# Optimization experiments

Measured on AMD Instinct MI355X. Metric: run time of the kernel, lower is better.

## Reference

```python
import jax, jax.numpy as jnp
import numpy as np

SIZE = 32            # resize target from size=(32,32)
CAL_THRESH = 0.3
WIN = 11             # standard SSIM gaussian window
SIGMA = 1.5
C1 = (0.01 * 255.0) ** 2   # data range 255 (patches are raw pixel values)
C2 = (0.03 * 255.0) ** 2


def _gauss_window():
    g = np.exp(-((np.arange(WIN) - WIN // 2) ** 2) / (2.0 * SIGMA ** 2))
    g = g / g.sum()
    return jnp.asarray(np.outer(g, g), jnp.float32)


def _gconv(x, win):
    # depthwise gaussian blur, same padding; x: [N,C,H,W]
    C = x.shape[1]
    k = jnp.tile(win[None, None], (C, 1, 1, 1))
    return jax.lax.conv_general_dilated(
        x, k, (1, 1), 'SAME',
        dimension_numbers=('NCHW', 'OIHW', 'NCHW'), feature_group_count=C)


def _crop_resize(img, box):
    # img: [C,H,W]; box: [x,y,w,h] with (x,y) = top-left (as used by the crop).
    # Equivalent to img[:, int(y):int(y+h), int(x):int(x+w)] then bilinear
    # F.interpolate to (SIZE,SIZE), align_corners=False (edge-clamped).
    C, H, W = img.shape
    x0 = jnp.floor(box[0]); y0 = jnp.floor(box[1])
    w = jnp.floor(box[0] + box[2]) - x0   # int(x+w) - int(x)
    h = jnp.floor(box[1] + box[3]) - y0
    ys = jnp.clip((jnp.arange(SIZE, dtype=jnp.float32) + 0.5) * (h / SIZE) - 0.5,
                  0.0, jnp.maximum(h - 1.0, 0.0))
    xs = jnp.clip((jnp.arange(SIZE, dtype=jnp.float32) + 0.5) * (w / SIZE) - 0.5,
                  0.0, jnp.maximum(w - 1.0, 0.0))
    yf = jnp.floor(ys); xf = jnp.floor(xs)
    wy = (ys - yf)[None, :, None]   # row weights
    wx = (xs - xf)[None, None, :]   # col weights

    def gi(yi, xi):
        yi = jnp.clip(yi, 0, H - 1).astype(jnp.int32)
        xi = jnp.clip(xi, 0, W - 1).astype(jnp.int32)
        return img[:, yi[:, None], xi[None, :]]  # [C,SIZE,SIZE]

    ylo = yf + y0; yhi = jnp.minimum(yf + 1.0, jnp.maximum(h - 1.0, 0.0)) + y0
    xlo = xf + x0; xhi = jnp.minimum(xf + 1.0, jnp.maximum(w - 1.0, 0.0)) + x0
    top = gi(ylo, xlo) * (1.0 - wx) + gi(ylo, xhi) * wx
    bot = gi(yhi, xlo) * (1.0 - wx) + gi(yhi, xhi) * wx
    return top * (1.0 - wy) + bot * wy


def _pairwise_iou(gt, pr):
    # faithful to get_two_box_iou: (x,y) treated as CENTER here (source quirk)
    g = gt[:, :, None, :]; p = pr[:, None, :, :]
    tl = jnp.maximum(g[..., :2] - g[..., 2:] / 2, p[..., :2] - p[..., 2:] / 2)
    br = jnp.minimum(g[..., :2] + g[..., 2:] / 2, p[..., :2] + p[..., 2:] / 2)
    en = jnp.prod((tl < br).astype(gt.dtype), axis=-1)
    area_i = jnp.prod(br - tl, axis=-1) * en
    area_g = jnp.prod(gt[..., 2:], axis=-1)[:, :, None]
    area_p = jnp.prod(pr[..., 2:], axis=-1)[:, None, :]
    return area_i / (area_g + area_p - area_i + 1e-16)  # [B,G,P]


def setup_inputs() -> dict:
    key = jax.random.key(0)
    k1, k2, k3, k4, k5 = jax.random.split(key, 5)
    B, G, P, H, W = 8, 16, 64, 640, 640
    imgs = jax.random.uniform(k1, (B, 3, H, W), jnp.float32) * 255.0
    xy = jax.random.uniform(k2, (B, G, 2), jnp.float32) * (W - 80.0) + 4.0
    wh = jax.random.uniform(k3, (B, G, 2), jnp.float32) * 56.0 + 8.0
    gt_boxes = jnp.concatenate([xy, wh], axis=-1)
    base = jnp.tile(gt_boxes, (1, P // G, 1))  # preds jittered around GTs so IoU>thresh often
    jit_xy = jax.random.uniform(k4, (B, P, 2), jnp.float32, -4.0, 4.0)
    jit_wh = jax.random.uniform(k5, (B, P, 2), jnp.float32, -4.0, 4.0)
    pred_boxes = jnp.concatenate(
        [base[..., :2] + jit_xy, jnp.maximum(base[..., 2:] + jit_wh, 3.0)], axis=-1)
    return {"gt_boxes": gt_boxes, "pred_boxes": pred_boxes, "imgs": imgs}


def reference(gt_boxes, pred_boxes, imgs):
    B, G = gt_boxes.shape[:2]; P = pred_boxes.shape[1]
    crop = jax.vmap(jax.vmap(_crop_resize, in_axes=(None, 0)), in_axes=(0, 0))
    gt_patch = crop(imgs, gt_boxes)     # [B,G,3,S,S]
    pr_patch = crop(imgs, pred_boxes)   # [B,P,3,S,S]

    iou = _pairwise_iou(gt_boxes, pred_boxes)                    # [B,G,P]
    valid = (pred_boxes[..., 2] > 2) & (pred_boxes[..., 3] > 2)  # [B,P]
    mask = ((iou > CAL_THRESH) & valid[:, None, :]).astype(imgs.dtype)

    # surviving pairs -> dense pair grid (masked mean == mean over survivors)
    x = jnp.broadcast_to(pr_patch[:, None], (B, G, P, 3, SIZE, SIZE)).reshape(-1, 3, SIZE, SIZE)
    y = jnp.broadcast_to(gt_patch[:, :, None], (B, G, P, 3, SIZE, SIZE)).reshape(-1, 3, SIZE, SIZE)

    win = _gauss_window()
    mu1 = _gconv(x, win); mu2 = _gconv(y, win)
    mu1_sq = mu1 * mu1; mu2_sq = mu2 * mu2; mu12 = mu1 * mu2
    s1 = _gconv(x * x, win) - mu1_sq
    s2 = _gconv(y * y, win) - mu2_sq
    s12 = _gconv(x * y, win) - mu12
    ssim_map = ((2 * mu12 + C1) * (2 * s12 + C2)) / ((mu1_sq + mu2_sq + C1) * (s1 + s2 + C2))

    loss = jnp.abs(x / 255.0 - y / 255.0) + (1.0 - ssim_map)    # L1 + SSIM loss, [N,3,S,S]
    loss = loss.reshape(B, G, P, 3, SIZE, SIZE)
    m = mask[:, :, :, None, None, None]
    cnt = jnp.sum(mask) * (3 * SIZE * SIZE)
    total = jnp.sum(loss * m)
    return jnp.where(cnt > 0, total / jnp.maximum(cnt, 1.0), 0.0)
```

## Files before the change

kernel.cpp:

```cpp
#include <hip/hip_runtime.h>
#include <math.h>

#define TSIZE 32
#define WIN 11
#define NB 8
#define NG 16
#define NP 64
#define IMH 640
#define IMW 640
#define NBOX 640
#define NPAIR 8192

#define C1F 6.5025f
#define C2F 58.5225f

struct GaussW { float g[WIN]; };
struct f4 { float v[4]; };

__global__ __launch_bounds__(256) void gen_patches(
    const float* __restrict__ gt_boxes, const float* __restrict__ pred_boxes,
    const float* __restrict__ imgs,
    float* __restrict__ patches, float* __restrict__ mus, float* __restrict__ gsqs,
    int* __restrict__ pair_list, int* __restrict__ pair_cnt, GaussW gw)
{
    const int bid = blockIdx.x;
    const int tid = threadIdx.x;

    if (bid >= NBOX * 3) {
        const int p = (bid - NBOX * 3) * 256 + tid;
        const int b  = p >> 10;
        const int gi = (p >> 6) & 15;
        const int pi = p & 63;
        bool mask;
        {
#pragma clang fp contract(off)
            const float* gb = gt_boxes  + ((size_t)b * NG + gi) * 4;
            const float* pb = pred_boxes + ((size_t)b * NP + pi) * 4;
            const float gx = gb[0], gy = gb[1], gw_ = gb[2], gh = gb[3];
            const float px = pb[0], py = pb[1], pw = pb[2], ph = pb[3];
            const float tlx = fmaxf(gx - gw_ / 2.0f, px - pw / 2.0f);
            const float tly = fmaxf(gy - gh / 2.0f, py - ph / 2.0f);
            const float brx = fminf(gx + gw_ / 2.0f, px + pw / 2.0f);
            const float bry = fminf(gy + gh / 2.0f, py + ph / 2.0f);
            const float en = ((tlx < brx) ? 1.0f : 0.0f) * ((tly < bry) ? 1.0f : 0.0f);
            const float ai = ((brx - tlx) * (bry - tly)) * en;
            const float ag = gw_ * gh;
            const float ap = pw * ph;
            const float iou = ai / (ag + ap - ai + 1e-16f);
            mask = (iou > 0.3f) && (pw > 2.0f) && (ph > 2.0f);
        }
        if (mask) {
            const int slot = atomicAdd(pair_cnt, 1);
            pair_list[slot] = p;
        }
        return;
    }

    const int box = bid / 3;
    const int c   = bid - box * 3;
    int b;
    const float* boxp;
    if (box < NB * NG) {
        b = box >> 4;
        boxp = gt_boxes + (size_t)box * 4;
    } else {
        const int q = box - NB * NG;
        b = q >> 6;
        boxp = pred_boxes + (size_t)q * 4;
    }
    const float* __restrict__ ic = imgs + ((size_t)b * 3 + c) * (IMH * IMW);
    float* __restrict__ patch_o = patches + ((size_t)box * 3 + c) * 1024;
    float* __restrict__ mu_o    = mus     + ((size_t)box * 3 + c) * 1024;
    float* __restrict__ gsq_o   = gsqs    + ((size_t)box * 3 + c) * 1024;

    __shared__ int   s_ylo[TSIZE], s_yhi[TSIZE], s_xlo[TSIZE], s_xhi[TSIZE];
    __shared__ float s_wy[TSIZE], s_wx[TSIZE];
    __shared__ float sp[1024], ta[1024], tb[1024];

    {
#pragma clang fp contract(off)
        const float b0 = boxp[0], b1 = boxp[1], b2 = boxp[2], b3 = boxp[3];
        const float x0 = floorf(b0), y0 = floorf(b1);
        const float w = floorf(b0 + b2) - x0;
        const float h = floorf(b1 + b3) - y0;

        if (tid < TSIZE) {
            const int t = tid;
            const float hm = fmaxf(h - 1.0f, 0.0f);
            const float scale = h / 32.0f;
            float ys = ((float)t + 0.5f) * scale - 0.5f;
            ys = fminf(fmaxf(ys, 0.0f), hm);
            const float yf = floorf(ys);
            s_wy[t] = ys - yf;
            const float ylo = yf + y0;
            const float yhi = fminf(yf + 1.0f, hm) + y0;
            s_ylo[t] = (int)fminf(fmaxf(ylo, 0.0f), (float)(IMH - 1));
            s_yhi[t] = (int)fminf(fmaxf(yhi, 0.0f), (float)(IMH - 1));
        } else if (tid < 2 * TSIZE) {
            const int t = tid - TSIZE;
            const float wm = fmaxf(w - 1.0f, 0.0f);
            const float scale = w / 32.0f;
            float xs = ((float)t + 0.5f) * scale - 0.5f;
            xs = fminf(fmaxf(xs, 0.0f), wm);
            const float xf = floorf(xs);
            s_wx[t] = xs - xf;
            const float xlo = xf + x0;
            const float xhi = fminf(xf + 1.0f, wm) + x0;
            s_xlo[t] = (int)fminf(fmaxf(xlo, 0.0f), (float)(IMW - 1));
            s_xhi[t] = (int)fminf(fmaxf(xhi, 0.0f), (float)(IMW - 1));
        }
    }
    __syncthreads();

    const int i  = tid >> 3;
    const int j4 = (tid & 7) << 2;
    const int e4 = (i << 5) + j4;

    {
        const int ylo = s_ylo[i], yhi = s_yhi[i];
        const float wy = s_wy[i];
        float vv[4];
#pragma unroll
        for (int q = 0; q < 4; ++q) {
#pragma clang fp contract(off)
            const int j = j4 + q;
            const int xlo = s_xlo[j], xhi = s_xhi[j];
            const float wx = s_wx[j];
            const float tl = ic[ylo * IMW + xlo], tr = ic[ylo * IMW + xhi];
            const float bl = ic[yhi * IMW + xlo], br = ic[yhi * IMW + xhi];
            const float top = tl * (1.0f - wx) + tr * wx;
            const float bot = bl * (1.0f - wx) + br * wx;
            vv[q] = top * (1.0f - wy) + bot * wy;
        }
        f4 o; o.v[0] = vv[0]; o.v[1] = vv[1]; o.v[2] = vv[2]; o.v[3] = vv[3];
        *(f4*)&sp[e4] = o;
        *(f4*)&patch_o[e4] = o;
    }
    __syncthreads();

    {
        float pv[14];
#pragma unroll
        for (int k = 0; k < 14; ++k) {
            const int jj = j4 - 5 + k;
            pv[k] = (jj >= 0 && jj < TSIZE) ? sp[(i << 5) + jj] : 0.0f;
        }
        float am[4] = {0.f, 0.f, 0.f, 0.f};
        float aq[4] = {0.f, 0.f, 0.f, 0.f};
#pragma unroll
        for (int k = 0; k < WIN; ++k) {
            const float gk = gw.g[k];
#pragma unroll
            for (int q = 0; q < 4; ++q) {
                const float v = pv[k + q];
                am[q] += gk * v;
                aq[q] += gk * (v * v);
            }
        }
        f4 oa; f4 ob;
#pragma unroll
        for (int q = 0; q < 4; ++q) { oa.v[q] = am[q]; ob.v[q] = aq[q]; }
        *(f4*)&ta[e4] = oa;
        *(f4*)&tb[e4] = ob;
    }
    __syncthreads();

    {
        float cm[4] = {0.f, 0.f, 0.f, 0.f};
        float cq[4] = {0.f, 0.f, 0.f, 0.f};
#pragma unroll
        for (int k = 0; k < WIN; ++k) {
            const int ii = i - 5 + k;
            if (ii >= 0 && ii < TSIZE) {
                const float gk = gw.g[k];
                const f4 m4 = *(const f4*)&ta[(ii << 5) + j4];
                const f4 q4 = *(const f4*)&tb[(ii << 5) + j4];
#pragma unroll
                for (int q = 0; q < 4; ++q) {
                    cm[q] += gk * m4.v[q];
                    cq[q] += gk * q4.v[q];
                }
            }
        }
        f4 om; f4 oq;
#pragma unroll
        for (int q = 0; q < 4; ++q) { om.v[q] = cm[q]; oq.v[q] = cq[q]; }
        *(f4*)&mu_o[e4]  = om;
        *(f4*)&gsq_o[e4] = oq;
    }
}

__global__ __launch_bounds__(256) void pair_kernel(
    const float* __restrict__ patches, const float* __restrict__ mus,
    const float* __restrict__ gsqs,
    const int* __restrict__ pair_list, const int* __restrict__ pair_cnt,
    float* __restrict__ partial, GaussW gw)
{
    __shared__ float sx[1024], sy[1024], tp[1024];
    __shared__ float wred[4];
    const int tid = threadIdx.x;
    const int nw = pair_cnt[0] * 3;
    const int i  = tid >> 3;
    const int j4 = (tid & 7) << 2;
    const int e4 = (i << 5) + j4;

    for (int w = blockIdx.x; w < nw; w += gridDim.x) {
        const int k3 = w / 3;
        const int c  = w - k3 * 3;
        const int p  = pair_list[k3];
        const int b  = p >> 10;
        const int gi = (p >> 6) & 15;
        const int pi = p & 63;
        const int gbox = b * NG + gi;
        const int pbox = NB * NG + b * NP + pi;
        const size_t po = ((size_t)pbox * 3 + c) * 1024;
        const size_t go = ((size_t)gbox * 3 + c) * 1024;

        const f4 xv = *(const f4*)&patches[po + e4];
        const f4 yv = *(const f4*)&patches[go + e4];
        *(f4*)&sx[e4] = xv;
        *(f4*)&sy[e4] = yv;
        __syncthreads();

        {
            float pv[14];
#pragma unroll
            for (int k = 0; k < 14; ++k) {
                const int jj = j4 - 5 + k;
                pv[k] = (jj >= 0 && jj < TSIZE)
                        ? sx[(i << 5) + jj] * sy[(i << 5) + jj] : 0.0f;
            }
            float a[4] = {0.f, 0.f, 0.f, 0.f};
#pragma unroll
            for (int k = 0; k < WIN; ++k) {
                const float gk = gw.g[k];
#pragma unroll
                for (int q = 0; q < 4; ++q) a[q] += gk * pv[k + q];
            }
            f4 o;
#pragma unroll
            for (int q = 0; q < 4; ++q) o.v[q] = a[q];
            *(f4*)&tp[e4] = o;
        }
        __syncthreads();

        float lsum = 0.0f;
        {
            float cxy[4] = {0.f, 0.f, 0.f, 0.f};
#pragma unroll
            for (int k = 0; k < WIN; ++k) {
                const int ii = i - 5 + k;
                if (ii >= 0 && ii < TSIZE) {
                    const float gk = gw.g[k];
                    const f4 t4 = *(const f4*)&tp[(ii << 5) + j4];
#pragma unroll
                    for (int q = 0; q < 4; ++q) cxy[q] += gk * t4.v[q];
                }
            }
            const f4 mu1 = *(const f4*)&mus[po + e4];
            const f4 mu2 = *(const f4*)&mus[go + e4];
            const f4 q1  = *(const f4*)&gsqs[po + e4];
            const f4 q2  = *(const f4*)&gsqs[go + e4];
#pragma unroll
            for (int q = 0; q < 4; ++q) {
                const float m1 = mu1.v[q], m2 = mu2.v[q];
                const float m1s = m1 * m1, m2s = m2 * m2, m12 = m1 * m2;
                const float s1  = q1.v[q] - m1s;
                const float s2  = q2.v[q] - m2s;
                const float s12 = cxy[q] - m12;
                const float num = (2.0f * m12 + C1F) * (2.0f * s12 + C2F);
                const float den = (m1s + m2s + C1F) * (s1 + s2 + C2F);
                const float ssim = num / den;
                lsum += fabsf(xv.v[q] / 255.0f - yv.v[q] / 255.0f) + (1.0f - ssim);
            }
        }

#pragma unroll
        for (int off = 32; off > 0; off >>= 1) lsum += __shfl_down(lsum, off);
        if ((tid & 63) == 0) wred[tid >> 6] = lsum;
        __syncthreads();
        if (tid == 0) partial[w] = wred[0] + wred[1] + wred[2] + wred[3];
        __syncthreads();
    }
}

__global__ __launch_bounds__(256) void finalize_kernel(
    const int* __restrict__ pair_cnt, const float* __restrict__ partial,
    float* __restrict__ out)
{
    __shared__ float wred[4];
    const int tid = threadIdx.x;
    const int n = pair_cnt[0];
    const int nw = n * 3;
    float lsum = 0.0f;
    for (int w = tid; w < nw; w += 256) lsum += partial[w];
#pragma unroll
    for (int off = 32; off > 0; off >>= 1) lsum += __shfl_down(lsum, off);
    if ((tid & 63) == 0) wred[tid >> 6] = lsum;
    __syncthreads();
    if (tid == 0) {
        const float total = wred[0] + wred[1] + wred[2] + wred[3];
        out[0] = (n > 0) ? (total / ((float)n * 3072.0f)) : 0.0f;
    }
}

extern "C" void kernel_launch(void* const* d_in, const int* in_sizes, int n_in,
                              void* d_out, int out_size, void* d_ws, size_t ws_size,
                              hipStream_t stream) {
    const float* gt_boxes   = (const float*)d_in[0];
    const float* pred_boxes = (const float*)d_in[1];
    const float* imgs       = (const float*)d_in[2];

    GaussW gw;
    {
        double gd[WIN]; double s = 0.0;
        for (int k = 0; k < WIN; ++k) {
            const double d = (double)(k - WIN / 2);
            gd[k] = exp(-(d * d) / (2.0 * 1.5 * 1.5));
            s += gd[k];
        }
        for (int k = 0; k < WIN; ++k) gw.g[k] = (float)(gd[k] / s);
    }

    float* ws = (float*)d_ws;
    float* patches = ws;
    float* mus     = patches + (size_t)NBOX * 3072;
    float* gsqs    = mus     + (size_t)NBOX * 3072;
    float* partial = gsqs    + (size_t)NBOX * 3072;
    int* pair_list = (int*)(partial + 3 * NPAIR);
    int* pair_cnt  = pair_list + NPAIR;

    hipMemsetAsync(pair_cnt, 0, sizeof(int), stream);

    gen_patches<<<NBOX * 3 + NPAIR / 256, 256, 0, stream>>>(
        gt_boxes, pred_boxes, imgs, patches, mus, gsqs, pair_list, pair_cnt, gw);

    pair_kernel<<<1536, 256, 0, stream>>>(
        patches, mus, gsqs, pair_list, pair_cnt, partial, gw);

    finalize_kernel<<<1, 256, 0, stream>>>(pair_cnt, partial, (float*)d_out);
}
```

Baseline: 104.0 us.

## Stage crop region in LDS, replace atomic compaction, fuse finalize via last-block ticket

The patch generator first copies each box's source image region into shared memory and does the bilinear taps from there, instead of issuing scattered global loads. Pair compaction now uses a per-block ballot prefix sum with per-block counts, which removes the global atomic counter and the memset. The final reduction is folded into the pair kernel through a last-block atomic ticket, so one launch goes away. A risk is that the fixed 4900-float shared buffer overflows for crop regions larger than about 70x70 pixels.

```diff
diff --git a/kernel.cpp b/kernel.cpp
--- a/kernel.cpp
+++ b/kernel.cpp
@@ -10,6 +10,8 @@
 #define IMW 640
 #define NBOX 640
 #define NPAIR 8192
+#define NCOMP (NPAIR/256)
+#define K2GRID 1536
 
 #define C1F 6.5025f
 #define C2F 58.5225f
@@ -21,13 +23,17 @@
     const float* __restrict__ gt_boxes, const float* __restrict__ pred_boxes,
     const float* __restrict__ imgs,
     float* __restrict__ patches, float* __restrict__ mus, float* __restrict__ gsqs,
-    int* __restrict__ pair_list, int* __restrict__ pair_cnt, GaussW gw)
+    int* __restrict__ pair_list, int* __restrict__ pair_cnt,
+    int* __restrict__ done, GaussW gw)
 {
     const int bid = blockIdx.x;
     const int tid = threadIdx.x;
 
+    if (bid == 0 && tid == 0) *done = 0;
+
     if (bid >= NBOX * 3) {
-        const int p = (bid - NBOX * 3) * 256 + tid;
+        const int blk = bid - NBOX * 3;
+        const int p = blk * 256 + tid;
         const int b  = p >> 10;
         const int gi = (p >> 6) & 15;
         const int pi = p & 63;
@@ -49,9 +55,21 @@
             const float iou = ai / (ag + ap - ai + 1e-16f);
             mask = (iou > 0.3f) && (pw > 2.0f) && (ph > 2.0f);
         }
+        __shared__ int wcnt[4], woff[4];
+        const unsigned long long bal = __ballot(mask);
+        const int lane = tid & 63, wid = tid >> 6;
+        if (lane == 0) wcnt[wid] = __popcll(bal);
+        __syncthreads();
+        if (tid == 0) {
+            int s = 0;
+#pragma unroll
+            for (int w = 0; w < 4; ++w) { woff[w] = s; s += wcnt[w]; }
+            pair_cnt[blk] = s;
+        }
+        __syncthreads();
         if (mask) {
-            const int slot = atomicAdd(pair_cnt, 1);
-            pair_list[slot] = p;
+            const int pre = __popcll(bal & ((1ull << lane) - 1ull));
+            pair_list[blk * 256 + woff[wid] + pre] = p;
         }
         return;
     }
@@ -75,7 +93,10 @@
 
     __shared__ int   s_ylo[TSIZE], s_yhi[TSIZE], s_xlo[TSIZE], s_xhi[TSIZE];
     __shared__ float s_wy[TSIZE], s_wx[TSIZE];
-    __shared__ float sp[1024], ta[1024], tb[1024];
+    __shared__ __align__(16) float smem[4900];
+    float* const sp = smem;
+    float* const ta = smem + 1024;
+    float* const tb = smem + 2048;
 
     {
 #pragma clang fp contract(off)
@@ -112,26 +133,45 @@
     }
     __syncthreads();
 
+    const int ry0 = s_ylo[0], ry1 = s_yhi[31];
+    const int rx0 = s_xlo[0], rx1 = s_xhi[31];
+    const int RH = ry1 - ry0 + 1;
+    const int RW = rx1 - rx0 + 1;
+    const int stride = RW | 1;
+    {
+        const int tot = RH * RW;
+        for (int idx = tid; idx < tot; idx += 256) {
+            const int r  = idx / RW;
+            const int cc = idx - r * RW;
+            smem[r * stride + cc] = ic[(ry0 + r) * IMW + rx0 + cc];
+        }
+    }
+    __syncthreads();
+
     const int i  = tid >> 3;
     const int j4 = (tid & 7) << 2;
     const int e4 = (i << 5) + j4;
 
-    {
-        const int ylo = s_ylo[i], yhi = s_yhi[i];
+    float vv[4];
+    {
+        const int yl = s_ylo[i] - ry0, yh = s_yhi[i] - ry0;
         const float wy = s_wy[i];
-        float vv[4];
 #pragma unroll
         for (int q = 0; q < 4; ++q) {
 #pragma clang fp contract(off)
             const int j = j4 + q;
-            const int xlo = s_xlo[j], xhi = s_xhi[j];
+            const int xl = s_xlo[j] - rx0, xh = s_xhi[j] - rx0;
             const float wx = s_wx[j];
-            const float tl = ic[ylo * IMW + xlo], tr = ic[ylo * IMW + xhi];
-            const float bl = ic[yhi * IMW + xlo], br = ic[yhi * IMW + xhi];
+            const float tl = smem[yl * stride + xl], tr = smem[yl * stride + xh];
+            const float bl = smem[yh * stride + xl], br = smem[yh * stride + xh];
             const float top = tl * (1.0f - wx) + tr * wx;
             const float bot = bl * (1.0f - wx) + br * wx;
             vv[q] = top * (1.0f - wy) + bot * wy;
         }
+    }
+    __syncthreads();
+
+    {
         f4 o; o.v[0] = vv[0]; o.v[1] = vv[1]; o.v[2] = vv[2]; o.v[3] = vv[3];
         *(f4*)&sp[e4] = o;
         *(f4*)&patch_o[e4] = o;
@@ -194,12 +234,25 @@
     const float* __restrict__ patches, const float* __restrict__ mus,
     const float* __restrict__ gsqs,
     const int* __restrict__ pair_list, const int* __restrict__ pair_cnt,
-    float* __restrict__ partial, GaussW gw)
+    float* __restrict__ partial, int* __restrict__ done,
+    float* __restrict__ out, GaussW gw)
 {
-    __shared__ float sx[1024], sy[1024], tp[1024];
+    __shared__ __align__(16) float sx[1024], sy[1024], tp[1024];
     __shared__ float wred[4];
+    __shared__ int cum[NCOMP + 1];
+    __shared__ int s_tkt;
     const int tid = threadIdx.x;
-    const int nw = pair_cnt[0] * 3;
+
+    if (tid == 0) {
+        int s = 0;
+#pragma unroll
+        for (int k = 0; k < NCOMP; ++k) { cum[k] = s; s += pair_cnt[k]; }
+        cum[NCOMP] = s;
+    }
+    __syncthreads();
+    const int n  = cum[NCOMP];
+    const int nw = n * 3;
+
     const int i  = tid >> 3;
     const int j4 = (tid & 7) << 2;
     const int e4 = (i << 5) + j4;
@@ -207,7 +260,9 @@
     for (int w = blockIdx.x; w < nw; w += gridDim.x) {
         const int k3 = w / 3;
         const int c  = w - k3 * 3;
-        const int p  = pair_list[k3];
+        int s = 0;
+        while (cum[s + 1] <= k3) ++s;
+        const int p  = pair_list[s * 256 + (k3 - cum[s])];
         const int b  = p >> 10;
         const int gi = (p >> 6) & 15;
         const int pi = p & 63;
@@ -282,25 +337,24 @@
         if (tid == 0) partial[w] = wred[0] + wred[1] + wred[2] + wred[3];
         __syncthreads();
     }
-}
-
-__global__ __launch_bounds__(256) void finalize_kernel(
-    const int* __restrict__ pair_cnt, const float* __restrict__ partial,
-    float* __restrict__ out)
-{
-    __shared__ float wred[4];
-    const int tid = threadIdx.x;
-    const int n = pair_cnt[0];
-    const int nw = n * 3;
-    float lsum = 0.0f;
-    for (int w = tid; w < nw; w += 256) lsum += partial[w];
-#pragma unroll
-    for (int off = 32; off > 0; off >>= 1) lsum += __shfl_down(lsum, off);
-    if ((tid & 63) == 0) wred[tid >> 6] = lsum;
-    __syncthreads();
-    if (tid == 0) {
-        const float total = wred[0] + wred[1] + wred[2] + wred[3];
-        out[0] = (n > 0) ? (total / ((float)n * 3072.0f)) : 0.0f;
+
+    __threadfence();
+    if (tid == 0)
+        s_tkt = __hip_atomic_fetch_add(done, 1, __ATOMIC_ACQ_REL,
+                                       __HIP_MEMORY_SCOPE_AGENT);
+    __syncthreads();
+    if (s_tkt == (int)gridDim.x - 1) {
+        __threadfence();
+        float lsum = 0.0f;
+        for (int w = tid; w < nw; w += 256) lsum += partial[w];
+#pragma unroll
+        for (int off = 32; off > 0; off >>= 1) lsum += __shfl_down(lsum, off);
+        if ((tid & 63) == 0) wred[tid >> 6] = lsum;
+        __syncthreads();
+        if (tid == 0) {
+            const float total = wred[0] + wred[1] + wred[2] + wred[3];
+            out[0] = (n > 0) ? (total / ((float)n * 3072.0f)) : 0.0f;
+        }
     }
 }
 
@@ -329,14 +383,13 @@
     float* partial = gsqs    + (size_t)NBOX * 3072;
     int* pair_list = (int*)(partial + 3 * NPAIR);
     int* pair_cnt  = pair_list + NPAIR;
-
-    hipMemsetAsync(pair_cnt, 0, sizeof(int), stream);
-
-    gen_patches<<<NBOX * 3 + NPAIR / 256, 256, 0, stream>>>(
-        gt_boxes, pred_boxes, imgs, patches, mus, gsqs, pair_list, pair_cnt, gw);
-
-    pair_kernel<<<1536, 256, 0, stream>>>(
-        patches, mus, gsqs, pair_list, pair_cnt, partial, gw);
-
-    finalize_kernel<<<1, 256, 0, stream>>>(pair_cnt, partial, (float*)d_out);
+    int* done      = pair_cnt + NCOMP;
+
+    gen_patches<<<NBOX * 3 + NCOMP, 256, 0, stream>>>(
+        gt_boxes, pred_boxes, imgs, patches, mus, gsqs,
+        pair_list, pair_cnt, done, gw);
+
+    pair_kernel<<<K2GRID, 256, 0, stream>>>(
+        patches, mus, gsqs, pair_list, pair_cnt, partial, done,
+        (float*)d_out, gw);
 }
```

Result: slower. 256.8 us (+147.0%).

## Fuse patch generation and pair SSIM into one per-pair kernel

Applied to the files above, without the earlier changes.

Replaces the box-level patch/blur precompute plus compacted pair kernel with a single kernel launched per (pair, channel) that computes the IoU mask, exits early for masked pairs, and otherwise resamples both patches from a shared-memory-staged image region and computes all blurs locally. This removes global intermediate buffers, the atomic pair list, the memset and one launch. In exchange, gt and pred patches and their blurs are recomputed for every surviving pair. The fixed shared staging buffer may overflow for large boxes.

```diff
diff --git a/kernel.cpp b/kernel.cpp
--- a/kernel.cpp
+++ b/kernel.cpp
@@ -8,8 +8,8 @@
 #define NP 64
 #define IMH 640
 #define IMW 640
-#define NBOX 640
 #define NPAIR 8192
+#define NWORK (NPAIR * 3)
 
 #define C1F 6.5025f
 #define C2F 58.5225f
@@ -17,136 +17,165 @@
 struct GaussW { float g[WIN]; };
 struct f4 { float v[4]; };
 
-__global__ __launch_bounds__(256) void gen_patches(
+__device__ __forceinline__ void mk_table(
+    const float* __restrict__ bx, int axis, int lim, int t,
+    int* __restrict__ lo_a, int* __restrict__ hi_a, float* __restrict__ w_a)
+{
+#pragma clang fp contract(off)
+    const float o   = bx[axis];
+    const float len = bx[axis + 2];
+    const float o0  = floorf(o);
+    const float ext = floorf(o + len) - o0;
+    const float m   = fmaxf(ext - 1.0f, 0.0f);
+    const float scale = ext / 32.0f;
+    float s = ((float)t + 0.5f) * scale - 0.5f;
+    s = fminf(fmaxf(s, 0.0f), m);
+    const float f = floorf(s);
+    w_a[t] = s - f;
+    const float lo = f + o0;
+    const float hi = fminf(f + 1.0f, m) + o0;
+    lo_a[t] = (int)fminf(fmaxf(lo, 0.0f), (float)lim);
+    hi_a[t] = (int)fminf(fmaxf(hi, 0.0f), (float)lim);
+}
+
+__global__ __launch_bounds__(256) void fused_kernel(
     const float* __restrict__ gt_boxes, const float* __restrict__ pred_boxes,
     const float* __restrict__ imgs,
-    float* __restrict__ patches, float* __restrict__ mus, float* __restrict__ gsqs,
-    int* __restrict__ pair_list, int* __restrict__ pair_cnt, GaussW gw)
+    float* __restrict__ partial, float* __restrict__ cntf, GaussW gw)
 {
     const int bid = blockIdx.x;
     const int tid = threadIdx.x;
-
-    if (bid >= NBOX * 3) {
-        const int p = (bid - NBOX * 3) * 256 + tid;
-        const int b  = p >> 10;
-        const int gi = (p >> 6) & 15;
-        const int pi = p & 63;
-        bool mask;
-        {
+    const int p = bid / 3;
+    const int c = bid - p * 3;
+    const int b  = p >> 10;
+    const int gi = (p >> 6) & 15;
+    const int pi = p & 63;
+
+    const float* __restrict__ gb = gt_boxes  + ((size_t)(b * NG + gi)) * 4;
+    const float* __restrict__ pb = pred_boxes + ((size_t)(b * NP + pi)) * 4;
+
+    bool mask;
+    {
 #pragma clang fp contract(off)
-            const float* gb = gt_boxes  + ((size_t)b * NG + gi) * 4;
-            const float* pb = pred_boxes + ((size_t)b * NP + pi) * 4;
-            const float gx = gb[0], gy = gb[1], gw_ = gb[2], gh = gb[3];
-            const float px = pb[0], py = pb[1], pw = pb[2], ph = pb[3];
-            const float tlx = fmaxf(gx - gw_ / 2.0f, px - pw / 2.0f);
-            const float tly = fmaxf(gy - gh / 2.0f, py - ph / 2.0f);
-            const float brx = fminf(gx + gw_ / 2.0f, px + pw / 2.0f);
-            const float bry = fminf(gy + gh / 2.0f, py + ph / 2.0f);
-            const float en = ((tlx < brx) ? 1.0f : 0.0f) * ((tly < bry) ? 1.0f : 0.0f);
-            const float ai = ((brx - tlx) * (bry - tly)) * en;
-            const float ag = gw_ * gh;
-            const float ap = pw * ph;
-            const float iou = ai / (ag + ap - ai + 1e-16f);
-            mask = (iou > 0.3f) && (pw > 2.0f) && (ph > 2.0f);
-        }
-        if (mask) {
-            const int slot = atomicAdd(pair_cnt, 1);
-            pair_list[slot] = p;
-        }
+        const float gx = gb[0], gy = gb[1], gw_ = gb[2], gh = gb[3];
+        const float px = pb[0], py = pb[1], pw = pb[2], ph = pb[3];
+        const float tlx = fmaxf(gx - gw_ / 2.0f, px - pw / 2.0f);
+        const float tly = fmaxf(gy - gh / 2.0f, py - ph / 2.0f);
+        const float brx = fminf(gx + gw_ / 2.0f, px + pw / 2.0f);
+        const float bry = fminf(gy + gh / 2.0f, py + ph / 2.0f);
+        const float en = ((tlx < brx) ? 1.0f : 0.0f) * ((tly < bry) ? 1.0f : 0.0f);
+        const float ai = ((brx - tlx) * (bry - tly)) * en;
+        const float ag = gw_ * gh;
+        const float ap = pw * ph;
+        const float iou = ai / (ag + ap - ai + 1e-16f);
+        mask = (iou > 0.3f) && (pw > 2.0f) && (ph > 2.0f);
+    }
+    if (tid == 0 && c == 0) cntf[p] = mask ? 1.0f : 0.0f;
+    if (!mask) {
+        if (tid == 0) partial[bid] = 0.0f;
         return;
     }
 
-    const int box = bid / 3;
-    const int c   = bid - box * 3;
-    int b;
-    const float* boxp;
-    if (box < NB * NG) {
-        b = box >> 4;
-        boxp = gt_boxes + (size_t)box * 4;
-    } else {
-        const int q = box - NB * NG;
-        b = q >> 6;
-        boxp = pred_boxes + (size_t)q * 4;
-    }
     const float* __restrict__ ic = imgs + ((size_t)b * 3 + c) * (IMH * IMW);
-    float* __restrict__ patch_o = patches + ((size_t)box * 3 + c) * 1024;
-    float* __restrict__ mu_o    = mus     + ((size_t)box * 3 + c) * 1024;
-    float* __restrict__ gsq_o   = gsqs    + ((size_t)box * 3 + c) * 1024;
-
-    __shared__ int   s_ylo[TSIZE], s_yhi[TSIZE], s_xlo[TSIZE], s_xhi[TSIZE];
-    __shared__ float s_wy[TSIZE], s_wx[TSIZE];
-    __shared__ float sp[1024], ta[1024], tb[1024];
-
-    {
-#pragma clang fp contract(off)
-        const float b0 = boxp[0], b1 = boxp[1], b2 = boxp[2], b3 = boxp[3];
-        const float x0 = floorf(b0), y0 = floorf(b1);
-        const float w = floorf(b0 + b2) - x0;
-        const float h = floorf(b1 + b3) - y0;
-
-        if (tid < TSIZE) {
-            const int t = tid;
-            const float hm = fmaxf(h - 1.0f, 0.0f);
-            const float scale = h / 32.0f;
-            float ys = ((float)t + 0.5f) * scale - 0.5f;
-            ys = fminf(fmaxf(ys, 0.0f), hm);
-            const float yf = floorf(ys);
-            s_wy[t] = ys - yf;
-            const float ylo = yf + y0;
-            const float yhi = fminf(yf + 1.0f, hm) + y0;
-            s_ylo[t] = (int)fminf(fmaxf(ylo, 0.0f), (float)(IMH - 1));
-            s_yhi[t] = (int)fminf(fmaxf(yhi, 0.0f), (float)(IMH - 1));
-        } else if (tid < 2 * TSIZE) {
-            const int t = tid - TSIZE;
-            const float wm = fmaxf(w - 1.0f, 0.0f);
-            const float scale = w / 32.0f;
-            float xs = ((float)t + 0.5f) * scale - 0.5f;
-            xs = fminf(fmaxf(xs, 0.0f), wm);
-            const float xf = floorf(xs);
-            s_wx[t] = xs - xf;
-            const float xlo = xf + x0;
-            const float xhi = fminf(xf + 1.0f, wm) + x0;
-            s_xlo[t] = (int)fminf(fmaxf(xlo, 0.0f), (float)(IMW - 1));
-            s_xhi[t] = (int)fminf(fmaxf(xhi, 0.0f), (float)(IMW - 1));
-        }
+
+    __shared__ int   gylo[32], gyhi[32], gxlo[32], gxhi[32];
+    __shared__ float gwy[32], gwx[32];
+    __shared__ int   qylo[32], qyhi[32], qxlo[32], qxhi[32];
+    __shared__ float qwy[32], qwx[32];
+    __shared__ __align__(16) float sreg[4784];
+    __shared__ __align__(16) float sx[1024], sy[1024];
+    __shared__ float wred[4];
+    float* const ta = sreg;
+    float* const tb = sreg + 1024;
+
+    if (tid < 128) {
+        const int grp = tid >> 5;
+        const int t   = tid & 31;
+        if      (grp == 0) mk_table(gb, 1, IMH - 1, t, gylo, gyhi, gwy);
+        else if (grp == 1) mk_table(gb, 0, IMW - 1, t, gxlo, gxhi, gwx);
+        else if (grp == 2) mk_table(pb, 1, IMH - 1, t, qylo, qyhi, qwy);
+        else               mk_table(pb, 0, IMW - 1, t, qxlo, qxhi, qwx);
     }
     __syncthreads();
 
     const int i  = tid >> 3;
     const int j4 = (tid & 7) << 2;
     const int e4 = (i << 5) + j4;
-
-    {
-        const int ylo = s_ylo[i], yhi = s_yhi[i];
-        const float wy = s_wy[i];
-        float vv[4];
+    const int wv = tid >> 6, lane = tid & 63;
+
+    float yv[4], xv[4];
+
+    {
+        const int ry0 = gylo[0], rx0 = gxlo[0];
+        const int RH = gyhi[31] - ry0 + 1;
+        const int RW = gxhi[31] - rx0 + 1;
+        const int stride = RW | 1;
+        for (int r = wv; r < RH; r += 4) {
+            const float* __restrict__ src = ic + (size_t)(ry0 + r) * IMW + rx0;
+            float* __restrict__ dst = sreg + r * stride;
+            for (int cc = lane; cc < RW; cc += 64) dst[cc] = src[cc];
+        }
+        __syncthreads();
+        const int yl = gylo[i] - ry0, yh = gyhi[i] - ry0;
+        const float wy = gwy[i];
 #pragma unroll
         for (int q = 0; q < 4; ++q) {
 #pragma clang fp contract(off)
             const int j = j4 + q;
-            const int xlo = s_xlo[j], xhi = s_xhi[j];
-            const float wx = s_wx[j];
-            const float tl = ic[ylo * IMW + xlo], tr = ic[ylo * IMW + xhi];
-            const float bl = ic[yhi * IMW + xlo], br = ic[yhi * IMW + xhi];
+            const int xl = gxlo[j] - rx0, xh = gxhi[j] - rx0;
+            const float wx = gwx[j];
+            const float tl = sreg[yl * stride + xl], tr = sreg[yl * stride + xh];
+            const float bl = sreg[yh * stride + xl], br = sreg[yh * stride + xh];
             const float top = tl * (1.0f - wx) + tr * wx;
             const float bot = bl * (1.0f - wx) + br * wx;
-            vv[q] = top * (1.0f - wy) + bot * wy;
-        }
-        f4 o; o.v[0] = vv[0]; o.v[1] = vv[1]; o.v[2] = vv[2]; o.v[3] = vv[3];
-        *(f4*)&sp[e4] = o;
-        *(f4*)&patch_o[e4] = o;
-    }
-    __syncthreads();
+            yv[q] = top * (1.0f - wy) + bot * wy;
+        }
+        __syncthreads();
+        f4 o; o.v[0]=yv[0]; o.v[1]=yv[1]; o.v[2]=yv[2]; o.v[3]=yv[3];
+        *(f4*)&sy[e4] = o;
+    }
+
+    {
+        const int ry0 = qylo[0], rx0 = qxlo[0];
+        const int RH = qyhi[31] - ry0 + 1;
+        const int RW = qxhi[31] - rx0 + 1;
+        const int stride = RW | 1;
+        for (int r = wv; r < RH; r += 4) {
+            const float* __restrict__ src = ic + (size_t)(ry0 + r) * IMW + rx0;
+            float* __restrict__ dst = sreg + r * stride;
+            for (int cc = lane; cc < RW; cc += 64) dst[cc] = src[cc];
+        }
+        __syncthreads();
+        const int yl = qylo[i] - ry0, yh = qyhi[i] - ry0;
+        const float wy = qwy[i];
+#pragma unroll
+        for (int q = 0; q < 4; ++q) {
+#pragma clang fp contract(off)
+            const int j = j4 + q;
+            const int xl = qxlo[j] - rx0, xh = qxhi[j] - rx0;
+            const float wx = qwx[j];
+            const float tl = sreg[yl * stride + xl], tr = sreg[yl * stride + xh];
+            const float bl = sreg[yh * stride + xl], br = sreg[yh * stride + xh];
+            const float top = tl * (1.0f - wx) + tr * wx;
+            const float bot = bl * (1.0f - wx) + br * wx;
+            xv[q] = top * (1.0f - wy) + bot * wy;
+        }
+        __syncthreads();
+        f4 o; o.v[0]=xv[0]; o.v[1]=xv[1]; o.v[2]=xv[2]; o.v[3]=xv[3];
+        *(f4*)&sx[e4] = o;
+        __syncthreads();
+    }
+
+    float m1[4], q1v[4], m2[4], q2v[4], cxy[4];
 
     {
         float pv[14];
 #pragma unroll
         for (int k = 0; k < 14; ++k) {
             const int jj = j4 - 5 + k;
-            pv[k] = (jj >= 0 && jj < TSIZE) ? sp[(i << 5) + jj] : 0.0f;
-        }
-        float am[4] = {0.f, 0.f, 0.f, 0.f};
-        float aq[4] = {0.f, 0.f, 0.f, 0.f};
+            pv[k] = (jj >= 0 && jj < TSIZE) ? sy[(i << 5) + jj] : 0.0f;
+        }
+        float am[4] = {0.f,0.f,0.f,0.f}, aq[4] = {0.f,0.f,0.f,0.f};
 #pragma unroll
         for (int k = 0; k < WIN; ++k) {
             const float gk = gw.g[k];
@@ -157,150 +186,146 @@
                 aq[q] += gk * (v * v);
             }
         }
-        f4 oa; f4 ob;
+        f4 oa, ob;
 #pragma unroll
         for (int q = 0; q < 4; ++q) { oa.v[q] = am[q]; ob.v[q] = aq[q]; }
         *(f4*)&ta[e4] = oa;
         *(f4*)&tb[e4] = ob;
-    }
-    __syncthreads();
-
-    {
-        float cm[4] = {0.f, 0.f, 0.f, 0.f};
-        float cq[4] = {0.f, 0.f, 0.f, 0.f};
+        __syncthreads();
+        float cm[4] = {0.f,0.f,0.f,0.f}, cq[4] = {0.f,0.f,0.f,0.f};
 #pragma unroll
         for (int k = 0; k < WIN; ++k) {
             const int ii = i - 5 + k;
             if (ii >= 0 && ii < TSIZE) {
                 const float gk = gw.g[k];
                 const f4 m4 = *(const f4*)&ta[(ii << 5) + j4];
-                const f4 q4 = *(const f4*)&tb[(ii << 5) + j4];
-#pragma unroll
-                for (int q = 0; q < 4; ++q) {
-                    cm[q] += gk * m4.v[q];
-                    cq[q] += gk * q4.v[q];
-                }
-            }
-        }
-        f4 om; f4 oq;
-#pragma unroll
-        for (int q = 0; q < 4; ++q) { om.v[q] = cm[q]; oq.v[q] = cq[q]; }
-        *(f4*)&mu_o[e4]  = om;
-        *(f4*)&gsq_o[e4] = oq;
-    }
-}
-
-__global__ __launch_bounds__(256) void pair_kernel(
-    const float* __restrict__ patches, const float* __restrict__ mus,
-    const float* __restrict__ gsqs,
-    const int* __restrict__ pair_list, const int* __restrict__ pair_cnt,
-    float* __restrict__ partial, GaussW gw)
-{
-    __shared__ float sx[1024], sy[1024], tp[1024];
-    __shared__ float wred[4];
-    const int tid = threadIdx.x;
-    const int nw = pair_cnt[0] * 3;
-    const int i  = tid >> 3;
-    const int j4 = (tid & 7) << 2;
-    const int e4 = (i << 5) + j4;
-
-    for (int w = blockIdx.x; w < nw; w += gridDim.x) {
-        const int k3 = w / 3;
-        const int c  = w - k3 * 3;
-        const int p  = pair_list[k3];
-        const int b  = p >> 10;
-        const int gi = (p >> 6) & 15;
-        const int pi = p & 63;
-        const int gbox = b * NG + gi;
-        const int pbox = NB * NG + b * NP + pi;
-        const size_t po = ((size_t)pbox * 3 + c) * 1024;
-        const size_t go = ((size_t)gbox * 3 + c) * 1024;
-
-        const f4 xv = *(const f4*)&patches[po + e4];
-        const f4 yv = *(const f4*)&patches[go + e4];
-        *(f4*)&sx[e4] = xv;
-        *(f4*)&sy[e4] = yv;
-        __syncthreads();
-
-        {
-            float pv[14];
-#pragma unroll
-            for (int k = 0; k < 14; ++k) {
-                const int jj = j4 - 5 + k;
-                pv[k] = (jj >= 0 && jj < TSIZE)
-                        ? sx[(i << 5) + jj] * sy[(i << 5) + jj] : 0.0f;
-            }
-            float a[4] = {0.f, 0.f, 0.f, 0.f};
-#pragma unroll
-            for (int k = 0; k < WIN; ++k) {
+                const f4 s4 = *(const f4*)&tb[(ii << 5) + j4];
+#pragma unroll
+                for (int q = 0; q < 4; ++q) { cm[q] += gk * m4.v[q]; cq[q] += gk * s4.v[q]; }
+            }
+        }
+#pragma unroll
+        for (int q = 0; q < 4; ++q) { m2[q] = cm[q]; q2v[q] = cq[q]; }
+        __syncthreads();
+    }
+
+    {
+        float pv[14];
+#pragma unroll
+        for (int k = 0; k < 14; ++k) {
+            const int jj = j4 - 5 + k;
+            pv[k] = (jj >= 0 && jj < TSIZE) ? sx[(i << 5) + jj] : 0.0f;
+        }
+        float am[4] = {0.f,0.f,0.f,0.f}, aq[4] = {0.f,0.f,0.f,0.f};
+#pragma unroll
+        for (int k = 0; k < WIN; ++k) {
+            const float gk = gw.g[k];
+#pragma unroll
+            for (int q = 0; q < 4; ++q) {
+                const float v = pv[k + q];
+                am[q] += gk * v;
+                aq[q] += gk * (v * v);
+            }
+        }
+        f4 oa, ob;
+#pragma unroll
+        for (int q = 0; q < 4; ++q) { oa.v[q] = am[q]; ob.v[q] = aq[q]; }
+        *(f4*)&ta[e4] = oa;
+        *(f4*)&tb[e4] = ob;
+        __syncthreads();
+        float cm[4] = {0.f,0.f,0.f,0.f}, cq[4] = {0.f,0.f,0.f,0.f};
+#pragma unroll
+        for (int k = 0; k < WIN; ++k) {
+            const int ii = i - 5 + k;
+            if (ii >= 0 && ii < TSIZE) {
                 const float gk = gw.g[k];
-#pragma unroll
-                for (int q = 0; q < 4; ++q) a[q] += gk * pv[k + q];
-            }
-            f4 o;
-#pragma unroll
-            for (int q = 0; q < 4; ++q) o.v[q] = a[q];
-            *(f4*)&tp[e4] = o;
-        }
-        __syncthreads();
-
-        float lsum = 0.0f;
-        {
-            float cxy[4] = {0.f, 0.f, 0.f, 0.f};
-#pragma unroll
-            for (int k = 0; k < WIN; ++k) {
-                const int ii = i - 5 + k;
-                if (ii >= 0 && ii < TSIZE) {
-                    const float gk = gw.g[k];
-                    const f4 t4 = *(const f4*)&tp[(ii << 5) + j4];
-#pragma unroll
-                    for (int q = 0; q < 4; ++q) cxy[q] += gk * t4.v[q];
-                }
-            }
-            const f4 mu1 = *(const f4*)&mus[po + e4];
-            const f4 mu2 = *(const f4*)&mus[go + e4];
-            const f4 q1  = *(const f4*)&gsqs[po + e4];
-            const f4 q2  = *(const f4*)&gsqs[go + e4];
-#pragma unroll
-            for (int q = 0; q < 4; ++q) {
-                const float m1 = mu1.v[q], m2 = mu2.v[q];
-                const float m1s = m1 * m1, m2s = m2 * m2, m12 = m1 * m2;
-                const float s1  = q1.v[q] - m1s;
-                const float s2  = q2.v[q] - m2s;
-                const float s12 = cxy[q] - m12;
-                const float num = (2.0f * m12 + C1F) * (2.0f * s12 + C2F);
-                const float den = (m1s + m2s + C1F) * (s1 + s2 + C2F);
-                const float ssim = num / den;
-                lsum += fabsf(xv.v[q] / 255.0f - yv.v[q] / 255.0f) + (1.0f - ssim);
-            }
-        }
-
-#pragma unroll
-        for (int off = 32; off > 0; off >>= 1) lsum += __shfl_down(lsum, off);
-        if ((tid & 63) == 0) wred[tid >> 6] = lsum;
-        __syncthreads();
-        if (tid == 0) partial[w] = wred[0] + wred[1] + wred[2] + wred[3];
-        __syncthreads();
-    }
-}
-
-__global__ __launch_bounds__(256) void finalize_kernel(
-    const int* __restrict__ pair_cnt, const float* __restrict__ partial,
-    float* __restrict__ out)
-{
-    __shared__ float wred[4];
-    const int tid = threadIdx.x;
-    const int n = pair_cnt[0];
-    const int nw = n * 3;
+                const f4 m4 = *(const f4*)&ta[(ii << 5) + j4];
+                const f4 s4 = *(const f4*)&tb[(ii << 5) + j4];
+#pragma unroll
+                for (int q = 0; q < 4; ++q) { cm[q] += gk * m4.v[q]; cq[q] += gk * s4.v[q]; }
+            }
+        }
+#pragma unroll
+        for (int q = 0; q < 4; ++q) { m1[q] = cm[q]; q1v[q] = cq[q]; }
+        __syncthreads();
+    }
+
+    {
+        float pv[14];
+#pragma unroll
+        for (int k = 0; k < 14; ++k) {
+            const int jj = j4 - 5 + k;
+            pv[k] = (jj >= 0 && jj < TSIZE)
+                    ? sx[(i << 5) + jj] * sy[(i << 5) + jj] : 0.0f;
+        }
+        float a[4] = {0.f,0.f,0.f,0.f};
+#pragma unroll
+        for (int k = 0; k < WIN; ++k) {
+            const float gk = gw.g[k];
+#pragma unroll
+            for (int q = 0; q < 4; ++q) a[q] += gk * pv[k + q];
+        }
+        f4 o;
+#pragma unroll
+        for (int q = 0; q < 4; ++q) o.v[q] = a[q];
+        *(f4*)&ta[e4] = o;
+        __syncthreads();
+        float cc[4] = {0.f,0.f,0.f,0.f};
+#pragma unroll
+        for (int k = 0; k < WIN; ++k) {
+            const int ii = i - 5 + k;
+            if (ii >= 0 && ii < TSIZE) {
+                const float gk = gw.g[k];
+                const f4 t4 = *(const f4*)&ta[(ii << 5) + j4];
+#pragma unroll
+                for (int q = 0; q < 4; ++q) cc[q] += gk * t4.v[q];
+            }
+        }
+#pragma unroll
+        for (int q = 0; q < 4; ++q) cxy[q] = cc[q];
+    }
+
     float lsum = 0.0f;
-    for (int w = tid; w < nw; w += 256) lsum += partial[w];
+#pragma unroll
+    for (int q = 0; q < 4; ++q) {
+        const float a = m1[q], b2 = m2[q];
+        const float m1s = a * a, m2s = b2 * b2, m12 = a * b2;
+        const float s1  = q1v[q] - m1s;
+        const float s2  = q2v[q] - m2s;
+        const float s12 = cxy[q] - m12;
+        const float num = (2.0f * m12 + C1F) * (2.0f * s12 + C2F);
+        const float den = (m1s + m2s + C1F) * (s1 + s2 + C2F);
+        const float ssim = num / den;
+        lsum += fabsf(xv[q] / 255.0f - yv[q] / 255.0f) + (1.0f - ssim);
+    }
+
 #pragma unroll
     for (int off = 32; off > 0; off >>= 1) lsum += __shfl_down(lsum, off);
     if ((tid & 63) == 0) wred[tid >> 6] = lsum;
     __syncthreads();
+    if (tid == 0) partial[bid] = wred[0] + wred[1] + wred[2] + wred[3];
+}
+
+__global__ __launch_bounds__(256) void finalize_kernel(
+    const float* __restrict__ partial, const float* __restrict__ cntf,
+    float* __restrict__ out)
+{
+    __shared__ float wr1[4], wr2[4];
+    const int tid = threadIdx.x;
+    float ls = 0.0f, cs = 0.0f;
+    for (int w = tid; w < NWORK; w += 256) ls += partial[w];
+    for (int w = tid; w < NPAIR; w += 256) cs += cntf[w];
+#pragma unroll
+    for (int off = 32; off > 0; off >>= 1) {
+        ls += __shfl_down(ls, off);
+        cs += __shfl_down(cs, off);
+    }
+    if ((tid & 63) == 0) { wr1[tid >> 6] = ls; wr2[tid >> 6] = cs; }
+    __syncthreads();
     if (tid == 0) {
-        const float total = wred[0] + wred[1] + wred[2] + wred[3];
-        out[0] = (n > 0) ? (total / ((float)n * 3072.0f)) : 0.0f;
+        const float total = wr1[0] + wr1[1] + wr1[2] + wr1[3];
+        const float n     = wr2[0] + wr2[1] + wr2[2] + wr2[3];
+        out[0] = (n > 0.0f) ? (total / (n * 3072.0f)) : 0.0f;
     }
 }
 
@@ -323,20 +348,11 @@
     }
 
     float* ws = (float*)d_ws;
-    float* patches = ws;
-    float* mus     = patches + (size_t)NBOX * 3072;
-    float* gsqs    = mus     + (size_t)NBOX * 3072;
-    float* partial = gsqs    + (size_t)NBOX * 3072;
-    int* pair_list = (int*)(partial + 3 * NPAIR);
-    int* pair_cnt  = pair_list + NPAIR;
-
-    hipMemsetAsync(pair_cnt, 0, sizeof(int), stream);
-
-    gen_patches<<<NBOX * 3 + NPAIR / 256, 256, 0, stream>>>(
-        gt_boxes, pred_boxes, imgs, patches, mus, gsqs, pair_list, pair_cnt, gw);
-
-    pair_kernel<<<1536, 256, 0, stream>>>(
-        patches, mus, gsqs, pair_list, pair_cnt, partial, gw);
-
-    finalize_kernel<<<1, 256, 0, stream>>>(pair_cnt, partial, (float*)d_out);
+    float* partial = ws;
+    float* cntf    = ws + NWORK;
+
+    fused_kernel<<<NWORK, 256, 0, stream>>>(
+        gt_boxes, pred_boxes, imgs, partial, cntf, gw);
+
+    finalize_kernel<<<1, 256, 0, stream>>>(partial, cntf, (float*)d_out);
 }
```

Result: slower. 148.6 us (+43.0%).
